# Kernel optimization log

Measured on AMD Instinct MI355X. Metric: run time of the kernel, lower is better.

## Reference

```python
import jax, jax.numpy as jnp
import numpy as np

N = 100000
E = 1600000
IN_DIM = 128
OUT_DIM = 128


def setup_inputs() -> dict:
    key = jax.random.key(0)
    k1, k2, k3, k4 = jax.random.split(key, 4)
    x = jax.random.normal(k1, (N, IN_DIM), dtype=jnp.float32)
    edge_index = jax.random.randint(k2, (2, E), 0, N, dtype=jnp.int64)
    # GCNConv linear weight [in, out] and bias [out]
    W = jax.random.normal(k3, (IN_DIM, OUT_DIM), dtype=jnp.float32) / np.sqrt(IN_DIM)
    b = jax.random.normal(k4, (OUT_DIM,), dtype=jnp.float32) * 0.01
    return {"x": x, "edge_index": edge_index, "W": W, "b": b}


def reference(x, edge_index, W, b):
    n = x.shape[0]
    # linear transform first (PyG GCNConv applies lin before propagate)
    h = x @ W  # [N, OUT_DIM]
    # add self-loops
    loops = jnp.arange(n, dtype=edge_index.dtype)
    src = jnp.concatenate([edge_index[0], loops])
    dst = jnp.concatenate([edge_index[1], loops])
    # symmetric degree normalization (degree counted on dst, incl. self-loops)
    deg = jnp.zeros((n,), dtype=h.dtype).at[dst].add(1.0)
    dinv = jnp.where(deg > 0, jax.lax.rsqrt(deg), 0.0)
    norm = dinv[src] * dinv[dst]  # [E+N]
    # gather, scale, scatter-sum
    msgs = h[src] * norm[:, None]  # [E+N, OUT_DIM]
    out = jax.ops.segment_sum(msgs, dst, num_segments=n) + b
    return jax.nn.relu(out)
```

## Files before the change

kernel.cpp:

```cpp
#include <hip/hip_runtime.h>
#include <cstdint>
#include <cstddef>

#define IN_DIM 128
#define OUT_DIM 128
#define NR 8
#define ACAP 448
#define NS 256
#define NSUB_MAX 64
#define LCAP 192
#define SBCAP 4864
#define SCAP 4864

typedef int vint4 __attribute__((ext_vector_type(4)));
typedef float vfloat2 __attribute__((ext_vector_type(2)));

__device__ __forceinline__ unsigned short f2bf(float f) {
  unsigned int u = __float_as_uint(f);
  u = (u + 0x7FFFu + ((u >> 16) & 1u)) >> 16;
  return (unsigned short)u;
}
__device__ __forceinline__ float bf_lo(unsigned int v) { return __uint_as_float(v << 16); }
__device__ __forceinline__ float bf_hi(unsigned int v) { return __uint_as_float(v & 0xFFFF0000u); }

__global__ void k_zero_i32(int* __restrict__ p, int n) {
  int i = blockIdx.x * blockDim.x + threadIdx.x;
  int st = gridDim.x * blockDim.x;
  for (; i < n; i += st) p[i] = 0;
}

__global__ void k_zero_f32(float* __restrict__ p, long long n) {
  long long i = (long long)blockIdx.x * blockDim.x + threadIdx.x;
  long long st = (long long)gridDim.x * blockDim.x;
  for (; i < n; i += st) p[i] = 0.0f;
}

__global__ void k_hist(const int* __restrict__ dst, int E, int* __restrict__ deg) {
  int i = blockIdx.x * blockDim.x + threadIdx.x;
  int st = gridDim.x * blockDim.x;
  for (; i < E; i += st) atomicAdd(&deg[dst[i]], 1);
}

__global__ void k_dinv(const int* __restrict__ deg, float* __restrict__ dinv, int n) {
  int i = blockIdx.x * blockDim.x + threadIdx.x;
  int st = gridDim.x * blockDim.x;
  for (; i < n; i += st) dinv[i] = rsqrtf((float)(deg[i] + 1));
}

__global__ __launch_bounds__(256) void k_bucket2(const int* __restrict__ ei, int E, int n,
                                                 unsigned int* __restrict__ bkt, int bcap,
                                                 int* __restrict__ bcnt,
                                                 int2* __restrict__ ovf, int* __restrict__ ocnt) {
  __shared__ unsigned int buf[NR][ACAP];
  __shared__ int cnt[NR];
  __shared__ int base[NR];
  const int rs = (n + NR - 1) / NR;
  const int tid = threadIdx.x;
  const int E4 = E >> 2;
  const vint4* s4 = (const vint4*)ei;
  const vint4* d4 = (const vint4*)(ei + E);
  const int nChunks = (E4 + 511) >> 9;

  for (int c = blockIdx.x; c < nChunks; c += gridDim.x) {
    if (tid < NR) cnt[tid] = 0;
    __syncthreads();
    const int i0 = c << 9;
#pragma unroll
    for (int u = 0; u < 2; ++u) {
      int i = i0 + (u << 8) + tid;
      if (i < E4) {
        vint4 s = __builtin_nontemporal_load(&s4[i]);
        vint4 d = __builtin_nontemporal_load(&d4[i]);
#define PUT(dd, ss)                                                                         \
        {                                                                                   \
          int rr = (dd) / rs;                                                               \
          unsigned int w = ((unsigned int)((dd) - rr * rs) << 17) | (unsigned int)(ss);     \
          int pos = atomicAdd(&cnt[rr], 1);                                                 \
          if (pos < ACAP) buf[rr][pos] = w;                                                 \
          else { int op = atomicAdd(ocnt, 1); ovf[op] = make_int2((ss), (dd)); }            \
        }
        PUT(d.x, s.x) PUT(d.y, s.y) PUT(d.z, s.z) PUT(d.w, s.w)
#undef PUT
      }
    }
    __syncthreads();
    if (tid < NR) {
      int m = cnt[tid]; if (m > ACAP) m = ACAP;
      base[tid] = atomicAdd(&bcnt[tid], m);
    }
    __syncthreads();
#pragma unroll
    for (int r = 0; r < NR; ++r) {
      int m = cnt[r]; if (m > ACAP) m = ACAP;
      int b = base[r];
      unsigned int* dp = bkt + (size_t)r * bcap;
      for (int j = tid; j < m; j += 256) {
        int idx = b + j;
        if (idx < bcap) __builtin_nontemporal_store(buf[r][j], &dp[idx]);
        else {
          unsigned int w = buf[r][j];
          int op = atomicAdd(ocnt, 1);
          ovf[op] = make_int2((int)(w & 0x1FFFFu), r * rs + (int)(w >> 17));
        }
      }
    }
    __syncthreads();
  }
  if (blockIdx.x == 0 && tid == 0) {
    for (int i = E4 << 2; i < E; ++i) {
      int s = ei[i], d = ei[E + i];
      int r = d / rs;
      int p = atomicAdd(&bcnt[r], 1);
      if (p < bcap) bkt[(size_t)r * bcap + p] = ((unsigned int)(d - r * rs) << 17) | (unsigned int)s;
      else { int op = atomicAdd(ocnt, 1); ovf[op] = make_int2(s, d); }
    }
  }
}

__global__ __launch_bounds__(256) void k_subbkt(const unsigned int* __restrict__ bkt, int bcap,
                                                const int* __restrict__ bcnt,
                                                unsigned int* __restrict__ sbkt,
                                                int* __restrict__ sbcnt, int nsub, int n,
                                                int2* __restrict__ ovf, int* __restrict__ ocnt) {
  __shared__ unsigned int buf[NSUB_MAX][LCAP];
  __shared__ int cnt[NSUB_MAX];
  __shared__ int base[NSUB_MAX];
  const int tid = threadIdx.x;
  const int r = blockIdx.x & 7;
  const int gblk = blockIdx.x >> 3;
  const int nblk = gridDim.x >> 3;
  const int rs = (n + NR - 1) / NR;
  int cr = bcnt[r]; if (cr > bcap) cr = bcap;
  const unsigned int* bp = bkt + (size_t)r * bcap;
  const int nChunks = (cr + 4095) >> 12;

  for (int c = gblk; c < nChunks; c += nblk) {
    for (int t = tid; t < nsub; t += 256) cnt[t] = 0;
    __syncthreads();
    const int i0 = c << 12;
    const int iend = min(i0 + 4096, cr);
    for (int i = i0 + tid; i < iend; i += 256) {
      unsigned int w = bp[i];
      int sub = (int)(w >> 25);
      int pos = atomicAdd(&cnt[sub], 1);
      if (pos < LCAP) buf[sub][pos] = w;
      else { int op = atomicAdd(ocnt, 1); ovf[op] = make_int2((int)(w & 0x1FFFFu), r * rs + (int)(w >> 17)); }
    }
    __syncthreads();
    for (int t = tid; t < nsub; t += 256) {
      int m = cnt[t]; if (m > LCAP) m = LCAP;
      base[t] = atomicAdd(&sbcnt[t * NR + r], m);
    }
    __syncthreads();
    for (int s = 0; s < nsub; ++s) {
      int m = cnt[s]; if (m > LCAP) m = LCAP;
      int b = base[s];
      unsigned int* dp = sbkt + (size_t)(s * NR + r) * SBCAP;
      for (int j = tid; j < m; j += 256) {
        int idx = b + j;
        if (idx < SBCAP) dp[idx] = buf[s][j];
        else {
          unsigned int w = buf[s][j];
          int op = atomicAdd(ocnt, 1);
          ovf[op] = make_int2((int)(w & 0x1FFFFu), r * rs + (int)(w >> 17));
        }
      }
    }
    __syncthreads();
  }
}

__global__ __launch_bounds__(256) void k_subsort2(const unsigned int* __restrict__ sbkt,
                                                  const int* __restrict__ sbcnt, int n,
                                                  int* __restrict__ csr, int* __restrict__ rs_start,
                                                  int* __restrict__ cur_end, float* __restrict__ dinv) {
  __shared__ unsigned int raw[SBCAP];
  __shared__ unsigned int srt[SBCAP];
  __shared__ int hist[NS];
  __shared__ int pref[NS];
  __shared__ int off[NS];
  const int tid = threadIdx.x;
  const int r = blockIdx.x & 7;
  const int sub = blockIdx.x >> 3;
  const int rs = (n + NR - 1) / NR;
  const int rsz = min(rs, n - r * rs);
  const int lo_dl = sub << 8;
  if (lo_dl >= rsz) return;
  const int nsn = min(NS, rsz - lo_dl);

  hist[tid] = 0;
  __syncthreads();

  int m = sbcnt[blockIdx.x]; if (m > SBCAP) m = SBCAP;
  const unsigned int* bp = sbkt + (size_t)blockIdx.x * SBCAP;
  for (int i = tid; i < m; i += 256) {
    unsigned int w = bp[i];
    raw[i] = w;
    atomicAdd(&hist[(int)(w >> 17) & (NS - 1)], 1);
  }
  __syncthreads();

  pref[tid] = hist[tid];
  __syncthreads();
  for (int o = 1; o < NS; o <<= 1) {
    int v = pref[tid] + ((tid >= o) ? pref[tid - o] : 0);
    __syncthreads();
    pref[tid] = v;
    __syncthreads();
  }
  off[tid] = pref[tid] - hist[tid];
  __syncthreads();

  for (int i = tid; i < m; i += 256) {
    unsigned int w = raw[i];
    int p = atomicAdd(&off[(int)(w >> 17) & (NS - 1)], 1);
    srt[p] = w & 0x1FFFFu;
  }
  __syncthreads();

  const int sbase = blockIdx.x * SCAP;
  for (int i = tid; i < m; i += 256) csr[sbase + i] = (int)srt[i];
  if (tid < nsn) {
    int node = r * rs + lo_dl + tid;
    rs_start[node] = sbase + pref[tid] - hist[tid];
    cur_end[node] = sbase + pref[tid];
    dinv[node] = rsqrtf((float)(hist[tid] + 1));
  }
}

__global__ void k_scatter_ovf(const int2* __restrict__ ovf, const int* __restrict__ ocnt,
                              int* __restrict__ cur_end, int* __restrict__ csr, int csr_total) {
  int m = *ocnt;
  for (int i = blockIdx.x * blockDim.x + threadIdx.x; i < m; i += gridDim.x * blockDim.x) {
    int2 e = ovf[i];
    int p = atomicAdd(&cur_end[e.y], 1);
    if (p >= 0 && p < csr_total) csr[p] = e.x;
  }
}

__global__ __launch_bounds__(256) void k_gemm_scale(const float* __restrict__ x, const float* __restrict__ W,
                                                    const float* __restrict__ dinv,
                                                    unsigned short* __restrict__ gb, int M) {
  __shared__ float xT[32][128];
  __shared__ float Ws[32][128];
  const int tid = threadIdx.x;
  const int tc = tid & 15;
  const int tr = tid >> 4;
  const int row0 = blockIdx.x * 128;
  const int lr = tid & 127;
  const int lk = (tid >> 7) * 16;

  float acc[8][8] = {};

  for (int k0 = 0; k0 < IN_DIM; k0 += 32) {
    int grow = row0 + lr;
    if (grow >= M) grow = M - 1;
    const float4* xp = (const float4*)(x + (size_t)grow * IN_DIM + k0 + lk);
    float4 a0 = xp[0], a1 = xp[1], a2 = xp[2], a3 = xp[3];
    const float4* wp = (const float4*)(W + (size_t)(k0 + (tid >> 3)) * OUT_DIM + (tid & 7) * 16);
    float4 w0 = wp[0], w1 = wp[1], w2 = wp[2], w3 = wp[3];

    __syncthreads();
    xT[lk + 0][lr] = a0.x;  xT[lk + 1][lr] = a0.y;  xT[lk + 2][lr] = a0.z;  xT[lk + 3][lr] = a0.w;
    xT[lk + 4][lr] = a1.x;  xT[lk + 5][lr] = a1.y;  xT[lk + 6][lr] = a1.z;  xT[lk + 7][lr] = a1.w;
    xT[lk + 8][lr] = a2.x;  xT[lk + 9][lr] = a2.y;  xT[lk + 10][lr] = a2.z; xT[lk + 11][lr] = a2.w;
    xT[lk + 12][lr] = a3.x; xT[lk + 13][lr] = a3.y; xT[lk + 14][lr] = a3.z; xT[lk + 15][lr] = a3.w;
    float4* wsp = (float4*)&Ws[tid >> 3][(tid & 7) * 16];
    wsp[0] = w0; wsp[1] = w1; wsp[2] = w2; wsp[3] = w3;
    __syncthreads();

#pragma unroll
    for (int k = 0; k < 32; ++k) {
      float xv[8], wv[8];
      *(float4*)&xv[0] = *(const float4*)&xT[k][tr * 8];
      *(float4*)&xv[4] = *(const float4*)&xT[k][tr * 8 + 4];
      *(float4*)&wv[0] = *(const float4*)&Ws[k][tc * 8];
      *(float4*)&wv[4] = *(const float4*)&Ws[k][tc * 8 + 4];
#pragma unroll
      for (int ii = 0; ii < 8; ++ii)
#pragma unroll
        for (int jj = 0; jj < 8; ++jj)
          acc[ii][jj] = fmaf(xv[ii], wv[jj], acc[ii][jj]);
    }
  }

#pragma unroll
  for (int ii = 0; ii < 8; ++ii) {
    int rr = row0 + tr * 8 + ii;
    if (rr < M) {
      float s = dinv[rr];
      uint4 o;
      o.x = (unsigned int)f2bf(acc[ii][0] * s) | ((unsigned int)f2bf(acc[ii][1] * s) << 16);
      o.y = (unsigned int)f2bf(acc[ii][2] * s) | ((unsigned int)f2bf(acc[ii][3] * s) << 16);
      o.z = (unsigned int)f2bf(acc[ii][4] * s) | ((unsigned int)f2bf(acc[ii][5] * s) << 16);
      o.w = (unsigned int)f2bf(acc[ii][6] * s) | ((unsigned int)f2bf(acc[ii][7] * s) << 16);
      *(uint4*)(gb + (size_t)rr * OUT_DIM + tc * 8) = o;
    }
  }
}

__global__ __launch_bounds__(256) void k_agg_se(const unsigned short* __restrict__ gb,
                                                const int* __restrict__ rs_start, const int* __restrict__ cur_end,
                                                const int* __restrict__ csr, const float* __restrict__ dinv,
                                                const float* __restrict__ bias, float* __restrict__ out, int n) {
  const int lane = threadIdx.x & 63;
  const int wave = __builtin_amdgcn_readfirstlane(threadIdx.x >> 6);
  const int wpb = blockDim.x >> 6;
  const int nWaves = gridDim.x * wpb;
  const int c2 = lane * 2;
  const float2 bb = *(const float2*)(bias + c2);

  for (int node = blockIdx.x * wpb + wave; node < n; node += nWaves) {
    const int s = rs_start[node];
    const int e = cur_end[node];
    unsigned int sv = *(const unsigned int*)(gb + (size_t)node * OUT_DIM + c2);
    float ax = bf_lo(sv), ay = bf_hi(sv);
    int i = s;
    for (; i + 8 <= e; i += 8) {
      int s0 = csr[i + 0], s1 = csr[i + 1], s2 = csr[i + 2], s3 = csr[i + 3];
      int s4 = csr[i + 4], s5 = csr[i + 5], s6 = csr[i + 6], s7 = csr[i + 7];
      unsigned int v0 = *(const unsigned int*)(gb + (size_t)s0 * OUT_DIM + c2);
      unsigned int v1 = *(const unsigned int*)(gb + (size_t)s1 * OUT_DIM + c2);
      unsigned int v2 = *(const unsigned int*)(gb + (size_t)s2 * OUT_DIM + c2);
      unsigned int v3 = *(const unsigned int*)(gb + (size_t)s3 * OUT_DIM + c2);
      unsigned int v4 = *(const unsigned int*)(gb + (size_t)s4 * OUT_DIM + c2);
      unsigned int v5 = *(const unsigned int*)(gb + (size_t)s5 * OUT_DIM + c2);
      unsigned int v6 = *(const unsigned int*)(gb + (size_t)s6 * OUT_DIM + c2);
      unsigned int v7 = *(const unsigned int*)(gb + (size_t)s7 * OUT_DIM + c2);
      ax += ((bf_lo(v0) + bf_lo(v1)) + (bf_lo(v2) + bf_lo(v3))) +
            ((bf_lo(v4) + bf_lo(v5)) + (bf_lo(v6) + bf_lo(v7)));
      ay += ((bf_hi(v0) + bf_hi(v1)) + (bf_hi(v2) + bf_hi(v3))) +
            ((bf_hi(v4) + bf_hi(v5)) + (bf_hi(v6) + bf_hi(v7)));
    }
    for (; i < e; ++i) {
      unsigned int v = *(const unsigned int*)(gb + (size_t)csr[i] * OUT_DIM + c2);
      ax += bf_lo(v);
      ay += bf_hi(v);
    }
    const float di = dinv[node];
    vfloat2 o;
    o.x = fmaxf(fmaf(ax, di, bb.x), 0.0f);
    o.y = fmaxf(fmaf(ay, di, bb.y), 0.0f);
    __builtin_nontemporal_store(o, (vfloat2*)(out + (size_t)node * OUT_DIM + c2));
  }
}

__global__ __launch_bounds__(256) void k_scatter(const int* __restrict__ ei, int E,
                                                 const unsigned short* __restrict__ gb, float* __restrict__ out) {
  const int lane = threadIdx.x & 63;
  const int wave = __builtin_amdgcn_readfirstlane(threadIdx.x >> 6);
  const int wpb = blockDim.x >> 6;
  const int nWaves = gridDim.x * wpb;
  const int c2 = lane * 2;
  for (int e = blockIdx.x * wpb + wave; e < E; e += nWaves) {
    int s = ei[e];
    int d = ei[E + e];
    unsigned int v = *(const unsigned int*)(gb + (size_t)s * OUT_DIM + c2);
    atomicAdd(&out[(size_t)d * OUT_DIM + c2 + 0], bf_lo(v));
    atomicAdd(&out[(size_t)d * OUT_DIM + c2 + 1], bf_hi(v));
  }
}

__global__ void k_finalize(const unsigned short* __restrict__ gb, const float* __restrict__ dinv,
                           const float* __restrict__ bias, float* __restrict__ out, int n) {
  int i = blockIdx.x * blockDim.x + threadIdx.x;
  int st = gridDim.x * blockDim.x;
  int total = n * OUT_DIM;
  for (; i < total; i += st) {
    int node = i >> 7;
    float gv = __uint_as_float(((unsigned int)gb[i]) << 16);
    float v = (out[i] + gv) * dinv[node] + bias[i & 127];
    out[i] = fmaxf(v, 0.0f);
  }
}

extern "C" void kernel_launch(void* const* d_in, const int* in_sizes, int n_in,
                              void* d_out, int out_size, void* d_ws, size_t ws_size,
                              hipStream_t stream) {
  const float* x = (const float*)d_in[0];
  const int* ei = (const int*)d_in[1];
  const float* W = (const float*)d_in[2];
  const float* bias = (const float*)d_in[3];
  float* out = (float*)d_out;

  const int N = in_sizes[0] / IN_DIM;
  const int E = in_sizes[1] / 2;

  const int rs = (N + NR - 1) / NR;
  const int nsub = (rs + NS - 1) / NS;
  const int nBlocksB = nsub * NR;
  const int csr_total = nBlocksB * SCAP;
  const int bcap = E / NR + E / 64 + 256;
  const int mBlocks = (N + 127) / 128;

  char* ws = (char*)d_ws;
  size_t off = 0;
  auto alloc = [&](size_t bytes) -> void* {
    void* p = ws + off;
    off += (bytes + 255) & ~(size_t)255;
    return p;
  };

  unsigned short* gb = (unsigned short*)alloc((size_t)N * OUT_DIM * sizeof(unsigned short));
  float* dinv = (float*)alloc((size_t)N * sizeof(float));
  int* rs_start = (int*)alloc((size_t)N * sizeof(int));
  int* cur_end = (int*)alloc((size_t)N * sizeof(int));
  int* csr = (int*)alloc((size_t)csr_total * sizeof(int));
  unsigned int* bkt = (unsigned int*)alloc((size_t)NR * bcap * sizeof(unsigned int));
  unsigned int* sbkt = (unsigned int*)alloc((size_t)nBlocksB * SBCAP * sizeof(unsigned int));
  int* sbcnt = (int*)alloc((size_t)nBlocksB * sizeof(int));
  int* bmeta = (int*)alloc(16 * sizeof(int));
  int2* ovf = (int2*)alloc((size_t)(E / 8 + 1024) * sizeof(int2));
  size_t bucket_need = off;

  const bool bucketed = (ws_size >= bucket_need) && (N <= (1 << 17)) && (rs <= (1 << 14)) &&
                        (nsub <= NSUB_MAX);

  if (bucketed) {
    k_zero_i32<<<1, 64, 0, stream>>>(bmeta, 16);
    k_zero_i32<<<1, 512, 0, stream>>>(sbcnt, nBlocksB);
    int aGrid = ((E >> 2) + 511) >> 9;
    if (aGrid < 1) aGrid = 1;
    k_bucket2<<<aGrid, 256, 0, stream>>>(ei, E, N, bkt, bcap, bmeta, ovf, bmeta + 8);
    k_subbkt<<<nBlocksB, 256, 0, stream>>>(bkt, bcap, bmeta, sbkt, sbcnt, nsub, N, ovf, bmeta + 8);
    k_subsort2<<<nBlocksB, 256, 0, stream>>>(sbkt, sbcnt, N, csr, rs_start, cur_end, dinv);
    k_gemm_scale<<<mBlocks, 256, 0, stream>>>(x, W, dinv, gb, N);
    k_scatter_ovf<<<64, 256, 0, stream>>>(ovf, bmeta + 8, cur_end, csr, csr_total);
    k_agg_se<<<2048, 256, 0, stream>>>(gb, rs_start, cur_end, csr, dinv, bias, out, N);
  } else {
    off = 0;
    unsigned short* gb2 = (unsigned short*)alloc((size_t)N * OUT_DIM * sizeof(unsigned short));
    int* deg = (int*)alloc((size_t)N * sizeof(int));
    float* dinv2 = (float*)alloc((size_t)N * sizeof(float));
    if (ws_size < off) return;
    k_zero_i32<<<256, 256, 0, stream>>>(deg, N);
    k_hist<<<2048, 256, 0, stream>>>(ei + E, E, deg);
    k_dinv<<<512, 256, 0, stream>>>(deg, dinv2, N);
    k_gemm_scale<<<mBlocks, 256, 0, stream>>>(x, W, dinv2, gb2, N);
    k_zero_f32<<<2048, 256, 0, stream>>>(out, (long long)N * OUT_DIM);
    k_scatter<<<4096, 256, 0, stream>>>(ei, E, gb2, out);
    k_finalize<<<2048, 256, 0, stream>>>(gb2, dinv2, bias, out, N);
  }
}
```

Measured before the change: 187.4 us.

## Replace FP32 SIMT GEMM with bf16 MFMA GEMM and fuse init kernels

```diff
diff --git a/kernel.cpp b/kernel.cpp
--- a/kernel.cpp
+++ b/kernel.cpp
@@ -14,6 +14,8 @@
 
 typedef int vint4 __attribute__((ext_vector_type(4)));
 typedef float vfloat2 __attribute__((ext_vector_type(2)));
+typedef short bf16x8 __attribute__((ext_vector_type(8)));
+typedef float f32x4 __attribute__((ext_vector_type(4)));
 
 __device__ __forceinline__ unsigned short f2bf(float f) {
   unsigned int u = __float_as_uint(f);
@@ -33,6 +35,18 @@
   long long i = (long long)blockIdx.x * blockDim.x + threadIdx.x;
   long long st = (long long)gridDim.x * blockDim.x;
   for (; i < n; i += st) p[i] = 0.0f;
+}
+
+__global__ void k_init(int* __restrict__ bmeta, int* __restrict__ sbcnt, int nB,
+                       const float* __restrict__ W, unsigned short* __restrict__ Wt_g) {
+  int gid = blockIdx.x * blockDim.x + threadIdx.x;
+  int st = gridDim.x * blockDim.x;
+  if (blockIdx.x == 0 && threadIdx.x < 16) bmeta[threadIdx.x] = 0;
+  for (int i = gid; i < nB; i += st) sbcnt[i] = 0;
+  for (int i = gid; i < IN_DIM * OUT_DIM; i += st) {
+    int k = i >> 7, c = i & 127;
+    Wt_g[c * IN_DIM + k] = f2bf(W[i]);
+  }
 }
 
 __global__ void k_hist(const int* __restrict__ dst, int E, int* __restrict__ deg) {
@@ -238,6 +252,65 @@
   }
 }
 
+__global__ __launch_bounds__(256) void k_gemm_mfma(const float* __restrict__ x,
+                                                   const unsigned short* __restrict__ Wt_g,
+                                                   const float* __restrict__ dinv,
+                                                   unsigned short* __restrict__ gb, int M) {
+  __shared__ unsigned short xT[64][136];
+  __shared__ unsigned short Wt[128][136];
+  const int tid = threadIdx.x;
+  const int row0 = blockIdx.x * 64;
+
+  for (int i = tid; i < (IN_DIM * OUT_DIM) / 8; i += 256) {
+    int c = i >> 4, k8 = (i & 15) * 8;
+    uint4 v = *(const uint4*)(Wt_g + (size_t)c * IN_DIM + k8);
+    *(uint4*)&Wt[c][k8] = v;
+  }
+  for (int i = tid; i < (64 * IN_DIM) / 4; i += 256) {
+    int idx = i * 4;
+    int r = idx >> 7, k = idx & 127;
+    int grow = row0 + r; if (grow >= M) grow = M - 1;
+    float4 v = *(const float4*)(x + (size_t)grow * IN_DIM + k);
+    ushort4 b;
+    b.x = f2bf(v.x); b.y = f2bf(v.y); b.z = f2bf(v.z); b.w = f2bf(v.w);
+    *(ushort4*)&xT[r][k] = b;
+  }
+  __syncthreads();
+
+  const int wv = tid >> 6;
+  const int lane = tid & 63;
+  const int l15 = lane & 15;
+  const int lk8 = (lane >> 4) * 8;
+
+  f32x4 acc[8];
+#pragma unroll
+  for (int ct = 0; ct < 8; ++ct) acc[ct] = (f32x4){0.f, 0.f, 0.f, 0.f};
+
+#pragma unroll
+  for (int kt = 0; kt < 4; ++kt) {
+    bf16x8 a = *(const bf16x8*)&xT[wv * 16 + l15][kt * 32 + lk8];
+#pragma unroll
+    for (int ct = 0; ct < 8; ++ct) {
+      bf16x8 b = *(const bf16x8*)&Wt[ct * 16 + l15][kt * 32 + lk8];
+      acc[ct] = __builtin_amdgcn_mfma_f32_16x16x32_bf16(a, b, acc[ct], 0, 0, 0);
+    }
+  }
+
+  const int drow0 = wv * 16 + (lane >> 4) * 4;
+#pragma unroll
+  for (int reg = 0; reg < 4; ++reg) {
+    int grow = row0 + drow0 + reg;
+    if (grow < M) {
+      float s = dinv[grow];
+      unsigned short* gp = gb + (size_t)grow * OUT_DIM + l15;
+#pragma unroll
+      for (int ct = 0; ct < 8; ++ct) {
+        gp[ct * 16] = f2bf(acc[ct][reg] * s);
+      }
+    }
+  }
+}
+
 __global__ __launch_bounds__(256) void k_gemm_scale(const float* __restrict__ x, const float* __restrict__ W,
                                                     const float* __restrict__ dinv,
                                                     unsigned short* __restrict__ gb, int M) {
@@ -271,16 +344,16 @@
 
 #pragma unroll
     for (int k = 0; k < 32; ++k) {
-      float xv[8], wv[8];
+      float xv[8], wvv[8];
       *(float4*)&xv[0] = *(const float4*)&xT[k][tr * 8];
       *(float4*)&xv[4] = *(const float4*)&xT[k][tr * 8 + 4];
-      *(float4*)&wv[0] = *(const float4*)&Ws[k][tc * 8];
-      *(float4*)&wv[4] = *(const float4*)&Ws[k][tc * 8 + 4];
+      *(float4*)&wvv[0] = *(const float4*)&Ws[k][tc * 8];
+      *(float4*)&wvv[4] = *(const float4*)&Ws[k][tc * 8 + 4];
 #pragma unroll
       for (int ii = 0; ii < 8; ++ii)
 #pragma unroll
         for (int jj = 0; jj < 8; ++jj)
-          acc[ii][jj] = fmaf(xv[ii], wv[jj], acc[ii][jj]);
+          acc[ii][jj] = fmaf(xv[ii], wvv[jj], acc[ii][jj]);
     }
   }
 
@@ -391,7 +464,7 @@
   const int nBlocksB = nsub * NR;
   const int csr_total = nBlocksB * SCAP;
   const int bcap = E / NR + E / 64 + 256;
-  const int mBlocks = (N + 127) / 128;
+  const int mBlocks64 = (N + 63) / 64;
 
   char* ws = (char*)d_ws;
   size_t off = 0;
@@ -409,6 +482,7 @@
   unsigned int* bkt = (unsigned int*)alloc((size_t)NR * bcap * sizeof(unsigned int));
   unsigned int* sbkt = (unsigned int*)alloc((size_t)nBlocksB * SBCAP * sizeof(unsigned int));
   int* sbcnt = (int*)alloc((size_t)nBlocksB * sizeof(int));
+  unsigned short* Wt_g = (unsigned short*)alloc((size_t)IN_DIM * OUT_DIM * sizeof(unsigned short));
   int* bmeta = (int*)alloc(16 * sizeof(int));
   int2* ovf = (int2*)alloc((size_t)(E / 8 + 1024) * sizeof(int2));
   size_t bucket_need = off;
@@ -417,14 +491,13 @@
                         (nsub <= NSUB_MAX);
 
   if (bucketed) {
-    k_zero_i32<<<1, 64, 0, stream>>>(bmeta, 16);
-    k_zero_i32<<<1, 512, 0, stream>>>(sbcnt, nBlocksB);
+    k_init<<<64, 256, 0, stream>>>(bmeta, sbcnt, nBlocksB, W, Wt_g);
     int aGrid = ((E >> 2) + 511) >> 9;
     if (aGrid < 1) aGrid = 1;
     k_bucket2<<<aGrid, 256, 0, stream>>>(ei, E, N, bkt, bcap, bmeta, ovf, bmeta + 8);
     k_subbkt<<<nBlocksB, 256, 0, stream>>>(bkt, bcap, bmeta, sbkt, sbcnt, nsub, N, ovf, bmeta + 8);
     k_subsort2<<<nBlocksB, 256, 0, stream>>>(sbkt, sbcnt, N, csr, rs_start, cur_end, dinv);
-    k_gemm_scale<<<mBlocks, 256, 0, stream>>>(x, W, dinv, gb, N);
+    k_gemm_mfma<<<mBlocks64, 256, 0, stream>>>(x, Wt_g, dinv, gb, N);
     k_scatter_ovf<<<64, 256, 0, stream>>>(ovf, bmeta + 8, cur_end, csr, csr_total);
     k_agg_se<<<2048, 256, 0, stream>>>(gb, rs_start, cur_end, csr, dinv, bias, out, N);
   } else {
@@ -436,7 +509,7 @@
     k_zero_i32<<<256, 256, 0, stream>>>(deg, N);
     k_hist<<<2048, 256, 0, stream>>>(ei + E, E, deg);
     k_dinv<<<512, 256, 0, stream>>>(deg, dinv2, N);
-    k_gemm_scale<<<mBlocks, 256, 0, stream>>>(x, W, dinv2, gb2, N);
+    k_gemm_scale<<<(N + 127) / 128, 256, 0, stream>>>(x, W, dinv2, gb2, N);
     k_zero_f32<<<2048, 256, 0, stream>>>(out, (long long)N * OUT_DIM);
     k_scatter<<<4096, 256, 0, stream>>>(ei, E, gb2, out);
     k_finalize<<<2048, 256, 0, stream>>>(gb2, dinv2, bias, out, N);
```

Result: faster. 152.7 us (-18.5%).
